# Optimization experiments

Measured on AMD Instinct MI355X. Metric: run time of the kernel, lower is better.

The kernel has to match this reference:

```python
import jax, jax.numpy as jnp
import numpy as np
import math

P, DD, N, E, NDRUGS = 256, 128, 1024, 250000, 200000
BASELINE = 6.0

def _prelu(x, a):
    return jnp.where(x >= 0, x, a * x)

def _lrelu(x):
    return jnp.where(x >= 0, x, 0.2 * x)

def _lin(x, W, b):
    return x @ W.T + b

def setup_inputs() -> dict:
    key = jax.random.key(0)
    ks = jax.random.split(key, 40)
    f32 = jnp.float32
    inp = {}
    inp["target_features"] = jax.random.normal(ks[0], (P,), f32)
    inp["form_features"] = jax.random.normal(ks[1], (N, P), f32)
    inp["role_features"] = jax.random.normal(ks[2], (N, P), f32)
    inp["form_neighbors"] = jnp.arange(N, dtype=jnp.int32)
    inp["form_binds_src"] = jax.random.randint(ks[3], (E,), 0, N, jnp.int32)
    inp["form_binds_dst"] = jax.random.randint(ks[4], (E,), 0, NDRUGS, jnp.int32)
    inp["form_binds_y"] = jax.random.uniform(ks[5], (E,), f32, 4.0, 9.0)
    inp["role_neighbors"] = jnp.arange(N, dtype=jnp.int32)
    inp["role_binds_src"] = jax.random.randint(ks[6], (E,), 0, N, jnp.int32)
    inp["role_binds_dst"] = jax.random.randint(ks[7], (E,), 0, NDRUGS, jnp.int32)
    inp["role_binds_y"] = jax.random.uniform(ks[8], (E,), f32, 4.0, 9.0)
    inp["drug_features"] = jax.random.normal(ks[9], (NDRUGS, DD), f32)
    s = 0.02
    # prot_refiner: Linear(P,P) -> PReLU -> Linear(P,P)
    inp["Wr1"] = jax.random.normal(ks[10], (P, P), f32) * s
    inp["br1"] = jnp.zeros((P,), f32)
    inp["ar1"] = jnp.asarray(0.25, f32)
    inp["Wr2"] = jax.random.normal(ks[11], (P, P), f32) * s
    inp["br2"] = jnp.zeros((P,), f32)
    # q/k/v projections
    inp["Wq"] = jax.random.normal(ks[12], (DD, P), f32) * s
    inp["bq"] = jnp.zeros((DD,), f32)
    inp["Wk"] = jax.random.normal(ks[13], (DD, DD), f32) * s
    inp["bk"] = jnp.zeros((DD,), f32)
    inp["Wv"] = jax.random.normal(ks[14], (DD, DD), f32) * s
    inp["bv"] = jnp.zeros((DD,), f32)
    inp["layer_emb"] = jax.random.normal(ks[15], (2, 16), f32) * s
    # attn_net: (2P+16)->128->64->1 with LeakyReLU(0.2)
    inp["Wa1"] = jax.random.normal(ks[16], (128, 2 * P + 16), f32) * s
    inp["ba1"] = jnp.zeros((128,), f32)
    inp["Wa2"] = jax.random.normal(ks[17], (64, 128), f32) * s
    inp["ba2"] = jnp.zeros((64,), f32)
    inp["Wa3"] = jax.random.normal(ks[18], (1, 64), f32) * s
    inp["ba3"] = jnp.zeros((1,), f32)
    # integration_mlp: Linear(DD,P) -> PReLU -> Linear(P,P)
    inp["Wi1"] = jax.random.normal(ks[19], (P, DD), f32) * s
    inp["bi1"] = jnp.zeros((P,), f32)
    inp["ai"] = jnp.asarray(0.25, f32)
    inp["Wi2"] = jax.random.normal(ks[20], (P, P), f32) * s
    inp["bi2"] = jnp.zeros((P,), f32)
    inp["ln_g"] = jnp.ones((P,), f32)
    inp["ln_b"] = jnp.zeros((P,), f32)
    return inp

def reference(target_features, form_features, role_features, form_neighbors,
              form_binds_src, form_binds_dst, form_binds_y,
              role_neighbors, role_binds_src, role_binds_dst, role_binds_y,
              drug_features,
              Wr1, br1, ar1, Wr2, br2, Wq, bq, Wk, bk, Wv, bv, layer_emb,
              Wa1, ba1, Wa2, ba2, Wa3, ba3, Wi1, bi1, ai, Wi2, bi2, ln_g, ln_b):
    def refine(x):
        return _lin(_prelu(_lin(x, Wr1, br1), ar1), Wr2, br2)

    zt = refine(target_features)          # [P]
    zf = refine(form_features)            # [N, P]
    zr = refine(role_features)            # [N, P]
    Qv = _lin(zt, Wq, bq)                 # [DD]

    def build_msgs(neighbors, src, dst, y):
        # segment id for each edge: position of src in (sorted) neighbor_ids;
        # edges whose src is not a neighbor go to the dummy segment n.
        n = neighbors.shape[0]
        pos = jnp.clip(jnp.searchsorted(neighbors, src), 0, n - 1)
        seg = jnp.where(neighbors[pos] == src, pos, n)
        d = drug_features[dst]                                # [E, DD] gather
        K = _lin(d, Wk, bk)                                   # [E, DD]
        V = _lin(d, Wv, bv) * (y - BASELINE)[:, None]         # [E, DD]
        s = (K @ Qv) / math.sqrt(DD)                          # [E]
        nseg = n + 1
        m = jax.ops.segment_max(s, seg, num_segments=nseg)    # per-neighbor max
        ex = jnp.exp(s - m[seg])                              # stable softmax numerator
        den = jax.ops.segment_sum(ex, seg, num_segments=nseg)[:n]          # [N]
        num = jax.ops.segment_sum(ex[:, None] * V, seg, num_segments=nseg)[:n]  # [N, DD]
        return jnp.where(den[:, None] > 0, num / jnp.maximum(den, 1e-30)[:, None], 0.0)

    form_msgs = build_msgs(form_neighbors, form_binds_src, form_binds_dst, form_binds_y)
    role_msgs = build_msgs(role_neighbors, role_binds_src, role_binds_dst, role_binds_y)

    def attn(zn, layer_id):
        n = zn.shape[0]
        le = jnp.broadcast_to(layer_emb[layer_id], (n, 16))
        zt_e = jnp.broadcast_to(zt, (n, P))
        x = jnp.concatenate([zt_e, zn, le], axis=-1)          # [N, 2P+16]
        h = _lrelu(_lin(x, Wa1, ba1))
        h = _lrelu(_lin(h, Wa2, ba2))
        return _lin(h, Wa3, ba3)                              # [N, 1]

    all_msgs = jnp.concatenate([form_msgs, role_msgs], axis=0)   # [2N, DD]
    all_attn = jnp.concatenate([attn(zf, 0), attn(zr, 1)], axis=0)  # [2N, 1]
    w = jax.nn.softmax(all_attn, axis=0)
    v_prior = jnp.sum(w * all_msgs, axis=0)                   # [DD]
    integ = _lin(_prelu(_lin(v_prior, Wi1, bi1), ai), Wi2, bi2)
    x = zt + integ
    mu = jnp.mean(x, axis=-1, keepdims=True)
    var = jnp.var(x, axis=-1, keepdims=True)
    z = (x - mu) / jnp.sqrt(var + 1e-5) * ln_g + ln_b
    return (z, form_msgs, role_msgs)
```

## Files before the change

kernel.cpp:

```cpp
#include <hip/hip_runtime.h>

#define NP 256
#define NDD 128
#define NN 1024
#define NE 250000
#define SB 62
#define RB 129

__global__ __launch_bounds__(256) void refine_qk_hist_kernel(
    const float* __restrict__ tgt, const float* __restrict__ formf, const float* __restrict__ rolef,
    const float* __restrict__ Wr1, const float* __restrict__ br1, const float* __restrict__ ar1,
    const float* __restrict__ Wr2, const float* __restrict__ br2,
    const float* __restrict__ Wq, const float* __restrict__ bq,
    const float* __restrict__ Wk, const float* __restrict__ bk,
    const int* __restrict__ neighF, const int* __restrict__ srcF,
    const int* __restrict__ neighR, const int* __restrict__ srcR,
    float* __restrict__ zt, float* __restrict__ zf, float* __restrict__ zr,
    float* __restrict__ qk, float* __restrict__ s0,
    int* __restrict__ count)
{
  __shared__ float X[16][NP];
  __shared__ float H[16][NP];
  __shared__ float Zs[NP];
  __shared__ float Q[NDD];
  __shared__ float red[NDD];
  const int t = threadIdx.x;

  if (blockIdx.x >= RB){
    int bi = blockIdx.x - RB;
    int role = bi >= SB ? 1 : 0;
    int blk = bi - role*SB;
    const int* neigh = role ? neighR : neighF;
    const int* src   = role ? srcR   : srcF;
    int* cnt = count + role*NN;
    int* NB = (int*)&X[0][0];
    int* lh = NB + NN;
    #pragma unroll
    for (int i = 0; i < NN/256; i++){
      NB[t + i*256] = neigh[t + i*256];
      lh[t + i*256] = 0;
    }
    __syncthreads();
    #pragma unroll
    for (int i = 0; i < 16; i++){
      int e = blk*4096 + i*256 + t;
      if (e < NE){
        int s = src[e];
        int pos;
        if ((unsigned)s < NN && NB[s] == s) pos = s;
        else {
          int lo = 0, hi = NN;
          while (lo < hi){ int mid = (lo+hi)>>1; if (NB[mid] < s) lo = mid+1; else hi = mid; }
          pos = lo < NN ? lo : NN-1;
        }
        if (NB[pos] == s) atomicAdd(&lh[pos], 1);
      }
    }
    __syncthreads();
    #pragma unroll
    for (int i = 0; i < NN/256; i++){
      int c = lh[t + i*256];
      if (c > 0) atomicAdd(&cnt[t + i*256], c);
    }
    return;
  }

  const int base = blockIdx.x * 16;
  #pragma unroll
  for (int r = 0; r < 16; r++){
    int row = base + r;
    if (row < 2*NN + 1){
      const float* xp;
      if (row == 0)        xp = tgt;
      else if (row <= NN)  xp = formf + (size_t)(row-1)*NP;
      else                 xp = rolef + (size_t)(row-NN-1)*NP;
      X[r][t] = xp[t];
    } else {
      X[r][t] = 0.f;
    }
  }
  __syncthreads();
  const float a1 = ar1[0];
  float acc[16];
  #pragma unroll
  for (int r = 0; r < 16; r++) acc[r] = 0.f;
  const float4* w1p = reinterpret_cast<const float4*>(Wr1) + t*(NP/4);
  for (int k4 = 0; k4 < NP/4; k4++){
    float4 w = w1p[k4];
    #pragma unroll
    for (int r = 0; r < 16; r++){
      float4 xv = *reinterpret_cast<const float4*>(&X[r][k4*4]);
      acc[r] = fmaf(w.x, xv.x, acc[r]);
      acc[r] = fmaf(w.y, xv.y, acc[r]);
      acc[r] = fmaf(w.z, xv.z, acc[r]);
      acc[r] = fmaf(w.w, xv.w, acc[r]);
    }
  }
  const float b1 = br1[t];
  #pragma unroll
  for (int r = 0; r < 16; r++){
    float h = acc[r] + b1;
    H[r][t] = h >= 0.f ? h : a1*h;
  }
  __syncthreads();
  #pragma unroll
  for (int r = 0; r < 16; r++) acc[r] = 0.f;
  const float4* w2p = reinterpret_cast<const float4*>(Wr2) + t*(NP/4);
  for (int k4 = 0; k4 < NP/4; k4++){
    float4 w = w2p[k4];
    #pragma unroll
    for (int r = 0; r < 16; r++){
      float4 hv = *reinterpret_cast<const float4*>(&H[r][k4*4]);
      acc[r] = fmaf(w.x, hv.x, acc[r]);
      acc[r] = fmaf(w.y, hv.y, acc[r]);
      acc[r] = fmaf(w.z, hv.z, acc[r]);
      acc[r] = fmaf(w.w, hv.w, acc[r]);
    }
  }
  const float b2 = br2[t];
  #pragma unroll
  for (int r = 0; r < 16; r++){
    int row = base + r;
    if (row < 2*NN + 1){
      float v = acc[r] + b2;
      float* op;
      if (row == 0){ op = zt; Zs[t] = v; }
      else if (row <= NN)  op = zf + (size_t)(row-1)*NP;
      else                 op = zr + (size_t)(row-NN-1)*NP;
      op[t] = v;
    }
  }

  if (blockIdx.x == 0){
    __syncthreads();
    if (t < NDD){
      float a = 0.f;
      const float4* wq = reinterpret_cast<const float4*>(Wq) + t*(NP/4);
      for (int k4 = 0; k4 < NP/4; k4++){
        float4 w = wq[k4];
        float4 zv = *reinterpret_cast<const float4*>(&Zs[k4*4]);
        a = fmaf(w.x, zv.x, fmaf(w.y, zv.y, fmaf(w.z, zv.z, fmaf(w.w, zv.w, a))));
      }
      float qv = a + bq[t];
      Q[t] = qv;
      red[t] = bk[t] * qv;
    }
    __syncthreads();
    const float rs = 0.08838834764831845f;
    if (t < NDD){
      float a2 = 0.f;
      for (int j = 0; j < NDD; j++) a2 = fmaf(Wk[j*NDD + t], Q[j], a2);
      qk[t] = a2 * rs;
    }
    for (int o = 64; o; o >>= 1){
      if (t < o) red[t] += red[t+o];
      __syncthreads();
    }
    if (t == 0) s0[0] = red[0] * rs;
  }
}

__device__ __forceinline__ int seg_of(const int* NB, int s){
  if ((unsigned)s < NN && NB[s] == s) return s;
  int lo = 0, hi = NN;
  while (lo < hi){ int mid = (lo+hi)>>1; if (NB[mid] < s) lo = mid+1; else hi = mid; }
  return lo < NN ? lo : NN-1;
}

__global__ __launch_bounds__(1024) void scatter_kernel(
    const int* __restrict__ neighF, const int* __restrict__ srcF,
    const int* __restrict__ dstF, const float* __restrict__ yF,
    const int* __restrict__ neighR, const int* __restrict__ srcR,
    const int* __restrict__ dstR, const float* __restrict__ yR,
    const int* __restrict__ count, int* __restrict__ cursor0,
    int* __restrict__ offsets, int2* __restrict__ edges)
{
  __shared__ int NB[NN];
  __shared__ int lcur[NN];
  __shared__ int sscan[NN];
  __shared__ int obase[NN];
  __shared__ int lbase[NN];
  int bi = blockIdx.x;
  int role = bi >= SB ? 1 : 0;
  int blk = bi - role*SB;
  const int* neigh = role ? neighR : neighF;
  const int* src   = role ? srcR   : srcF;
  const int* dst   = role ? dstR   : dstF;
  const float* yb  = role ? yR     : yF;
  int* cur0 = cursor0 + role*NN;
  int2* ed  = edges   + (size_t)role*NE;
  int t = threadIdx.x;
  NB[t] = neigh[t];
  lcur[t] = 0;
  int c0 = count[role*NN + t];
  sscan[t] = c0;
  __syncthreads();
  for (int o = 1; o < NN; o <<= 1){
    int v = (t >= o) ? sscan[t-o] : 0;
    __syncthreads();
    sscan[t] += v;
    __syncthreads();
  }
  obase[t] = sscan[t] - c0;
  if (blk == 0) offsets[role*NN + t] = sscan[t] - c0;
  __syncthreads();

  int segr[4], locr[4]; int2 edr[4];
  #pragma unroll
  for (int i = 0; i < 4; i++){
    int e = blk*4096 + i*1024 + t;
    segr[i] = -1;
    if (e < NE){
      int s = src[e];
      int pos = seg_of(NB, s);
      if (NB[pos] == s){
        segr[i] = pos;
        edr[i]  = make_int2(dst[e], __float_as_int(yb[e]));
        locr[i] = atomicAdd(&lcur[pos], 1);
      }
    }
  }
  __syncthreads();
  int c = lcur[t];
  if (c > 0) lbase[t] = obase[t] + atomicAdd(&cur0[t], c);
  __syncthreads();
  #pragma unroll
  for (int i = 0; i < 4; i++){
    if (segr[i] >= 0){
      ed[(size_t)(lbase[segr[i]] + locr[i])] = edr[i];
    }
  }
}

__global__ __launch_bounds__(256) void seg_kernel(
    const float* __restrict__ drug,
    const int2* __restrict__ edges,
    const int* __restrict__ offsets, const int* __restrict__ count,
    const float* __restrict__ qk, const float* __restrict__ s0p,
    float* __restrict__ g, float* __restrict__ den, float* __restrict__ cfac)
{
  int b = blockIdx.x;
  int tid = threadIdx.x;
  int w = tid >> 6, lane = tid & 63, l32 = lane & 31, half = lane >> 5;
  int off = offsets[b], cnt = count[b];
  int l = b >> 10;
  const int2* eb = edges + (size_t)l*NE;
  float4 q = reinterpret_cast<const float4*>(qk)[l32];
  float s0 = s0p[0];
  int chunk = (cnt + 3) >> 2;
  int start = w*chunk;
  int end = min(start + chunk, cnt);
  float dn = 0.f, cc = 0.f;
  float4 ga = make_float4(0.f,0.f,0.f,0.f);
  for (int i = start; i < end; i += 8){
    int dstp[4]; float yp[4]; bool vp[4];
    #pragma unroll
    for (int p2 = 0; p2 < 4; p2++){
      int idx = i + 2*p2 + half;
      bool v = idx < end;
      int2 e = eb[off + (v ? idx : start)];
      dstp[p2] = e.x; yp[p2] = __int_as_float(e.y); vp[p2] = v;
    }
    float4 dv[4];
    #pragma unroll
    for (int p2 = 0; p2 < 4; p2++){
      dv[p2] = reinterpret_cast<const float4*>(drug + (size_t)dstp[p2]*NDD)[l32];
    }
    #pragma unroll
    for (int p2 = 0; p2 < 4; p2++){
      float4 d = dv[p2];
      float s = fmaf(d.x, q.x, fmaf(d.y, q.y, fmaf(d.z, q.z, d.w*q.w)));
      s += __shfl_xor(s, 16, 64);
      s += __shfl_xor(s,  8, 64);
      s += __shfl_xor(s,  4, 64);
      s += __shfl_xor(s,  2, 64);
      s += __shfl_xor(s,  1, 64);
      float ex = vp[p2] ? __expf(s + s0) : 0.f;
      float wv = ex * (yp[p2] - 6.0f);
      dn += ex; cc += wv;
      ga.x = fmaf(wv, d.x, ga.x);
      ga.y = fmaf(wv, d.y, ga.y);
      ga.z = fmaf(wv, d.z, ga.z);
      ga.w = fmaf(wv, d.w, ga.w);
    }
  }
  __shared__ float4 sG[8][32];
  __shared__ float sD[8], sC[8];
  int slot = w*2 + half;
  sG[slot][l32] = ga;
  if (l32 == 0){ sD[slot] = dn; sC[slot] = cc; }
  __syncthreads();
  if (tid < NDD){
    int a = tid >> 2, c = tid & 3;
    float v = 0.f;
    #pragma unroll
    for (int k = 0; k < 8; k++)
      v += reinterpret_cast<const float*>(&sG[k][a])[c];
    g[(size_t)b*NDD + tid] = v;
    if (tid == 0){
      float ds = 0.f, cs = 0.f;
      #pragma unroll
      for (int k = 0; k < 8; k++){ ds += sD[k]; cs += sC[k]; }
      den[b] = ds; cfac[b] = cs;
    }
  }
}

__global__ __launch_bounds__(256) void attn_msgs_kernel(
    const float* __restrict__ zt, const float* __restrict__ zf, const float* __restrict__ zr,
    const float* __restrict__ lemb,
    const float* __restrict__ Wa1, const float* __restrict__ ba1,
    const float* __restrict__ Wa2, const float* __restrict__ ba2,
    const float* __restrict__ Wa3, const float* __restrict__ ba3,
    const float* __restrict__ g, const float* __restrict__ den, const float* __restrict__ cfac,
    const float* __restrict__ Wv, const float* __restrict__ bv,
    float* __restrict__ attn, float* __restrict__ msgsf, float* __restrict__ outm)
{
  int t = threadIdx.x;
  int tt = t & 127, grp = t >> 7;
  if (blockIdx.x < 256){
    __shared__ float X[8][528];
    __shared__ float H1[8][NDD];
    int base = blockIdx.x*8;
    for (int r = 0; r < 8; r++){
      int i = base + r;
      int layer = i >> 10, nn = i & (NN-1);
      const float* zn = (layer == 0) ? (zf + (size_t)nn*NP) : (zr + (size_t)nn*NP);
      for (int idx = t; idx < 528; idx += 256){
        float v;
        if (idx < NP)        v = zt[idx];
        else if (idx < 2*NP) v = zn[idx - NP];
        else                 v = lemb[layer*16 + (idx - 2*NP)];
        X[r][idx] = v;
      }
    }
    __syncthreads();
    float acc[4];
    #pragma unroll
    for (int r = 0; r < 4; r++) acc[r] = 0.f;
    const float4* w1 = reinterpret_cast<const float4*>(Wa1) + tt*(528/4);
    for (int k4 = 0; k4 < 132; k4++){
      float4 w = w1[k4];
      #pragma unroll
      for (int r = 0; r < 4; r++){
        float4 xv = *reinterpret_cast<const float4*>(&X[grp*4 + r][k4*4]);
        acc[r] = fmaf(w.x, xv.x, acc[r]);
        acc[r] = fmaf(w.y, xv.y, acc[r]);
        acc[r] = fmaf(w.z, xv.z, acc[r]);
        acc[r] = fmaf(w.w, xv.w, acc[r]);
      }
    }
    float b1 = ba1[tt];
    #pragma unroll
    for (int r = 0; r < 4; r++){
      float h = acc[r] + b1;
      H1[grp*4 + r][tt] = h >= 0.f ? h : 0.2f*h;
    }
    __syncthreads();
    if (tt < 64){
      float acc2[4];
      #pragma unroll
      for (int r = 0; r < 4; r++) acc2[r] = 0.f;
      const float4* w2 = reinterpret_cast<const float4*>(Wa2) + tt*(NDD/4);
      for (int k4 = 0; k4 < NDD/4; k4++){
        float4 w = w2[k4];
        #pragma unroll
        for (int r = 0; r < 4; r++){
          float4 hv = *reinterpret_cast<const float4*>(&H1[grp*4 + r][k4*4]);
          acc2[r] = fmaf(w.x, hv.x, acc2[r]);
          acc2[r] = fmaf(w.y, hv.y, acc2[r]);
          acc2[r] = fmaf(w.z, hv.z, acc2[r]);
          acc2[r] = fmaf(w.w, hv.w, acc2[r]);
        }
      }
      float b2 = ba2[tt];
      float w3 = Wa3[tt];
      float b3 = ba3[0];
      #pragma unroll
      for (int r = 0; r < 4; r++){
        float h = acc2[r] + b2;
        h = h >= 0.f ? h : 0.2f*h;
        float p = w3 * h;
        #pragma unroll
        for (int o = 32; o; o >>= 1) p += __shfl_xor(p, o, 64);
        if (tt == 0) attn[base + grp*4 + r] = p + b3;
      }
    }
  } else {
    __shared__ float G[8][NDD];
    int base = (blockIdx.x - 256)*8;
    #pragma unroll
    for (int r = 0; r < 4; r++) G[grp*4 + r][tt] = g[(size_t)(base + grp*4 + r)*NDD + tt];
    __syncthreads();
    float acc[4];
    #pragma unroll
    for (int r = 0; r < 4; r++) acc[r] = 0.f;
    const float4* wv4 = reinterpret_cast<const float4*>(Wv) + tt*(NDD/4);
    for (int k4 = 0; k4 < NDD/4; k4++){
      float4 w = wv4[k4];
      #pragma unroll
      for (int r = 0; r < 4; r++){
        float4 gv = *reinterpret_cast<const float4*>(&G[grp*4 + r][k4*4]);
        acc[r] = fmaf(w.x, gv.x, acc[r]);
        acc[r] = fmaf(w.y, gv.y, acc[r]);
        acc[r] = fmaf(w.z, gv.z, acc[r]);
        acc[r] = fmaf(w.w, gv.w, acc[r]);
      }
    }
    float bvj = bv[tt];
    #pragma unroll
    for (int r = 0; r < 4; r++){
      int row = base + grp*4 + r;
      float dn = den[row];
      float v = 0.f;
      if (dn > 0.f) v = (acc[r] + bvj*cfac[row]) / fmaxf(dn, 1e-30f);
      msgsf[(size_t)row*NDD + tt] = v;
      outm [(size_t)row*NDD + tt] = v;
    }
  }
}

__global__ __launch_bounds__(1024) void vprior_final_kernel(
    const float* __restrict__ attn, const float* __restrict__ msgsf,
    const float* __restrict__ zt,
    const float* __restrict__ Wi1, const float* __restrict__ bi1, const float* __restrict__ ai,
    const float* __restrict__ Wi2, const float* __restrict__ bi2,
    const float* __restrict__ ln_g, const float* __restrict__ ln_b,
    float* __restrict__ zout)
{
  __shared__ float A[2*NN];
  __shared__ float red[1024];
  __shared__ float Pp[8][NDD];
  __shared__ float V[NDD];
  __shared__ float T1[NP];
  __shared__ float red2[NP];
  int t = threadIdx.x;
  A[t] = attn[t]; A[t+1024] = attn[t+1024];
  __syncthreads();
  float mx = fmaxf(A[t], A[t+1024]);
  red[t] = mx; __syncthreads();
  for (int o = 512; o; o >>= 1){ if (t < o) red[t] = fmaxf(red[t], red[t+o]); __syncthreads(); }
  float M = red[0]; __syncthreads();
  float sm = __expf(A[t] - M) + __expf(A[t+1024] - M);
  red[t] = sm; __syncthreads();
  for (int o = 512; o; o >>= 1){ if (t < o) red[t] += red[t+o]; __syncthreads(); }
  float inv = 1.f / red[0]; __syncthreads();
  A[t]      = __expf(A[t]      - M) * inv;
  A[t+1024] = __expf(A[t+1024] - M) * inv;
  __syncthreads();
  int j = t & 127, grp = t >> 7;
  float acc = 0.f;
  int i0 = grp * 256;
  for (int i = i0; i < i0 + 256; i++) acc = fmaf(A[i], msgsf[(size_t)i*NDD + j], acc);
  Pp[grp][j] = acc;
  __syncthreads();
  if (t < NDD){
    float v = 0.f;
    #pragma unroll
    for (int gg = 0; gg < 8; gg++) v += Pp[gg][t];
    V[t] = v;
  }
  __syncthreads();
  float x = 0.f;
  if (t < NP){
    float a1 = 0.f;
    const float4* w1 = reinterpret_cast<const float4*>(Wi1) + t*(NDD/4);
    for (int k4 = 0; k4 < NDD/4; k4++){
      float4 w = w1[k4];
      float4 vv = *reinterpret_cast<const float4*>(&V[k4*4]);
      a1 = fmaf(w.x, vv.x, fmaf(w.y, vv.y, fmaf(w.z, vv.z, fmaf(w.w, vv.w, a1))));
    }
    float h = a1 + bi1[t];
    float a = ai[0];
    T1[t] = h >= 0.f ? h : a*h;
  }
  __syncthreads();
  if (t < NP){
    float a2 = 0.f;
    const float4* w2 = reinterpret_cast<const float4*>(Wi2) + t*(NP/4);
    for (int k4 = 0; k4 < NP/4; k4++){
      float4 w = w2[k4];
      float4 hv = *reinterpret_cast<const float4*>(&T1[k4*4]);
      a2 = fmaf(w.x, hv.x, fmaf(w.y, hv.y, fmaf(w.z, hv.z, fmaf(w.w, hv.w, a2))));
    }
    x = zt[t] + a2 + bi2[t];
    red2[t] = x;
  }
  __syncthreads();
  for (int o = 128; o; o >>= 1){ if (t < o) red2[t] += red2[t+o]; __syncthreads(); }
  float mu = red2[0] * (1.f/256.f); __syncthreads();
  float d = x - mu;
  if (t < NP) red2[t] = d*d;
  __syncthreads();
  for (int o = 128; o; o >>= 1){ if (t < o) red2[t] += red2[t+o]; __syncthreads(); }
  if (t < NP){
    float var = red2[0] * (1.f/256.f);
    float zz = d * rsqrtf(var + 1e-5f) * ln_g[t] + ln_b[t];
    zout[t] = zz;
  }
}

extern "C" void kernel_launch(void* const* d_in, const int* in_sizes, int n_in,
                              void* d_out, int out_size, void* d_ws, size_t ws_size,
                              hipStream_t stream)
{
  const float* tgt    = (const float*)d_in[0];
  const float* formf  = (const float*)d_in[1];
  const float* rolef  = (const float*)d_in[2];
  const int* fneigh   = (const int*)d_in[3];
  const int* fsrc     = (const int*)d_in[4];
  const int* fdst     = (const int*)d_in[5];
  const float* fy     = (const float*)d_in[6];
  const int* rneigh   = (const int*)d_in[7];
  const int* rsrc     = (const int*)d_in[8];
  const int* rdst     = (const int*)d_in[9];
  const float* ry     = (const float*)d_in[10];
  const float* drug   = (const float*)d_in[11];
  const float* Wr1 = (const float*)d_in[12];
  const float* br1 = (const float*)d_in[13];
  const float* ar1 = (const float*)d_in[14];
  const float* Wr2 = (const float*)d_in[15];
  const float* br2 = (const float*)d_in[16];
  const float* Wq  = (const float*)d_in[17];
  const float* bq  = (const float*)d_in[18];
  const float* Wk  = (const float*)d_in[19];
  const float* bk  = (const float*)d_in[20];
  const float* Wv  = (const float*)d_in[21];
  const float* bv  = (const float*)d_in[22];
  const float* lemb= (const float*)d_in[23];
  const float* Wa1 = (const float*)d_in[24];
  const float* ba1 = (const float*)d_in[25];
  const float* Wa2 = (const float*)d_in[26];
  const float* ba2 = (const float*)d_in[27];
  const float* Wa3 = (const float*)d_in[28];
  const float* ba3 = (const float*)d_in[29];
  const float* Wi1 = (const float*)d_in[30];
  const float* bi1 = (const float*)d_in[31];
  const float* ai  = (const float*)d_in[32];
  const float* Wi2 = (const float*)d_in[33];
  const float* bi2 = (const float*)d_in[34];
  const float* lng = (const float*)d_in[35];
  const float* lnb = (const float*)d_in[36];
  (void)in_sizes; (void)n_in; (void)out_size; (void)ws_size;

  float* ws = (float*)d_ws;
  float* zt_     = ws + 0;
  float* zf_     = ws + 256;
  float* zr_     = ws + 262400;
  float* qk_     = ws + 524544;
  float* s0_     = ws + 524672;
  float* attn_   = ws + 524800;
  float* den_    = ws + 527104;
  float* cfac_   = ws + 529152;
  float* g_      = ws + 531200;
  float* msgsf_  = ws + 793344;
  int*   count_  = (int*)(ws + 1055488);
  int*   offs_   = (int*)(ws + 1057536);
  int*   cursor_ = (int*)(ws + 1059584);
  int2*  edges_  = (int2*)(ws + 1061632);

  hipMemsetAsync(count_, 0, 3*2*NN*sizeof(int), stream);

  refine_qk_hist_kernel<<<RB + 2*SB, 256, 0, stream>>>(
      tgt, formf, rolef, Wr1, br1, ar1, Wr2, br2, Wq, bq, Wk, bk,
      fneigh, fsrc, rneigh, rsrc,
      zt_, zf_, zr_, qk_, s0_, count_);

  scatter_kernel<<<2*SB, 1024, 0, stream>>>(fneigh, fsrc, fdst, fy,
                                            rneigh, rsrc, rdst, ry,
                                            count_, cursor_, offs_, edges_);

  seg_kernel<<<2*NN, 256, 0, stream>>>(drug, edges_, offs_, count_, qk_, s0_,
                                       g_, den_, cfac_);

  attn_msgs_kernel<<<512, 256, 0, stream>>>(zt_, zf_, zr_, lemb,
                                            Wa1, ba1, Wa2, ba2, Wa3, ba3,
                                            g_, den_, cfac_, Wv, bv,
                                            attn_, msgsf_, (float*)d_out + NP);
  vprior_final_kernel<<<1, 1024, 0, stream>>>(attn_, msgsf_, zt_,
                                              Wi1, bi1, ai, Wi2, bi2,
                                              lng, lnb, (float*)d_out);
}
```

Measured before the change: 390.8 us.

## Transpose weights in a prep kernel and hoist constant attention-input terms

```diff
diff --git a/kernel.cpp b/kernel.cpp
--- a/kernel.cpp
+++ b/kernel.cpp
@@ -5,29 +5,66 @@
 #define NN 1024
 #define NE 250000
 #define SB 62
-#define RB 129
+#define RB2 257
+
+__global__ __launch_bounds__(256) void prep_kernel(
+    const float* __restrict__ Wr1, const float* __restrict__ Wr2,
+    const float* __restrict__ Wa1, const float* __restrict__ Wa2,
+    const float* __restrict__ Wv,
+    float* __restrict__ Wr1T, float* __restrict__ Wr2T,
+    float* __restrict__ Wa1mT, float* __restrict__ Wa2T, float* __restrict__ WvT)
+{
+  __shared__ float T[64][65];
+  int b = blockIdx.x, t = threadIdx.x;
+  const float* src; float* dst;
+  int sC, sr0, sc0, dC, dr0, dc0;
+  if (b < 16){        int ti=b;    src=Wr1; sC=256; sr0=(ti/4)*64; sc0=(ti%4)*64;
+                      dst=Wr1T; dC=256; dr0=sc0; dc0=sr0; }
+  else if (b < 32){   int ti=b-16; src=Wr2; sC=256; sr0=(ti/4)*64; sc0=(ti%4)*64;
+                      dst=Wr2T; dC=256; dr0=sc0; dc0=sr0; }
+  else if (b < 40){   int ti=b-32; src=Wa1; sC=528; sr0=(ti/4)*64; sc0=256+(ti%4)*64;
+                      dst=Wa1mT; dC=128; dr0=(ti%4)*64; dc0=sr0; }
+  else if (b < 42){   int ti=b-40; src=Wa2; sC=128; sr0=0; sc0=ti*64;
+                      dst=Wa2T; dC=64; dr0=sc0; dc0=0; }
+  else {              int ti=b-42; src=Wv;  sC=128; sr0=(ti/2)*64; sc0=(ti%2)*64;
+                      dst=WvT; dC=128; dr0=sc0; dc0=sr0; }
+  #pragma unroll
+  for (int j = 0; j < 16; j++){
+    int idx = t + j*256;
+    int r = idx >> 6, c = idx & 63;
+    T[c][r] = src[(size_t)(sr0 + r)*sC + sc0 + c];
+  }
+  __syncthreads();
+  #pragma unroll
+  for (int j = 0; j < 16; j++){
+    int idx = t + j*256;
+    int r = idx >> 6, c = idx & 63;
+    dst[(size_t)(dr0 + r)*dC + dc0 + c] = T[r][c];
+  }
+}
 
 __global__ __launch_bounds__(256) void refine_qk_hist_kernel(
     const float* __restrict__ tgt, const float* __restrict__ formf, const float* __restrict__ rolef,
-    const float* __restrict__ Wr1, const float* __restrict__ br1, const float* __restrict__ ar1,
-    const float* __restrict__ Wr2, const float* __restrict__ br2,
+    const float* __restrict__ Wr1T, const float* __restrict__ br1, const float* __restrict__ ar1,
+    const float* __restrict__ Wr2T, const float* __restrict__ br2,
     const float* __restrict__ Wq, const float* __restrict__ bq,
     const float* __restrict__ Wk, const float* __restrict__ bk,
+    const float* __restrict__ Wa1, const float* __restrict__ ba1, const float* __restrict__ lemb,
     const int* __restrict__ neighF, const int* __restrict__ srcF,
     const int* __restrict__ neighR, const int* __restrict__ srcR,
     float* __restrict__ zt, float* __restrict__ zf, float* __restrict__ zr,
-    float* __restrict__ qk, float* __restrict__ s0,
+    float* __restrict__ qk, float* __restrict__ s0, float* __restrict__ cl,
     int* __restrict__ count)
 {
-  __shared__ float X[16][NP];
-  __shared__ float H[16][NP];
+  __shared__ float X[8][NP];
+  __shared__ float H[8][NP];
   __shared__ float Zs[NP];
   __shared__ float Q[NDD];
   __shared__ float red[NDD];
   const int t = threadIdx.x;
 
-  if (blockIdx.x >= RB){
-    int bi = blockIdx.x - RB;
+  if (blockIdx.x >= RB2){
+    int bi = blockIdx.x - RB2;
     int role = bi >= SB ? 1 : 0;
     int blk = bi - role*SB;
     const int* neigh = role ? neighR : neighF;
@@ -65,9 +102,9 @@
     return;
   }
 
-  const int base = blockIdx.x * 16;
-  #pragma unroll
-  for (int r = 0; r < 16; r++){
+  const int base = blockIdx.x * 8;
+  #pragma unroll
+  for (int r = 0; r < 8; r++){
     int row = base + r;
     if (row < 2*NN + 1){
       const float* xp;
@@ -81,45 +118,49 @@
   }
   __syncthreads();
   const float a1 = ar1[0];
-  float acc[16];
-  #pragma unroll
-  for (int r = 0; r < 16; r++) acc[r] = 0.f;
-  const float4* w1p = reinterpret_cast<const float4*>(Wr1) + t*(NP/4);
-  for (int k4 = 0; k4 < NP/4; k4++){
-    float4 w = w1p[k4];
-    #pragma unroll
-    for (int r = 0; r < 16; r++){
-      float4 xv = *reinterpret_cast<const float4*>(&X[r][k4*4]);
-      acc[r] = fmaf(w.x, xv.x, acc[r]);
-      acc[r] = fmaf(w.y, xv.y, acc[r]);
-      acc[r] = fmaf(w.z, xv.z, acc[r]);
-      acc[r] = fmaf(w.w, xv.w, acc[r]);
+  float acc[8];
+  #pragma unroll
+  for (int r = 0; r < 8; r++) acc[r] = 0.f;
+  for (int k = 0; k < NP; k += 4){
+    float w0 = Wr1T[(k+0)*NP + t];
+    float w1 = Wr1T[(k+1)*NP + t];
+    float w2 = Wr1T[(k+2)*NP + t];
+    float w3 = Wr1T[(k+3)*NP + t];
+    #pragma unroll
+    for (int r = 0; r < 8; r++){
+      float4 x = *reinterpret_cast<const float4*>(&X[r][k]);
+      acc[r] = fmaf(w0, x.x, acc[r]);
+      acc[r] = fmaf(w1, x.y, acc[r]);
+      acc[r] = fmaf(w2, x.z, acc[r]);
+      acc[r] = fmaf(w3, x.w, acc[r]);
     }
   }
   const float b1 = br1[t];
   #pragma unroll
-  for (int r = 0; r < 16; r++){
+  for (int r = 0; r < 8; r++){
     float h = acc[r] + b1;
     H[r][t] = h >= 0.f ? h : a1*h;
   }
   __syncthreads();
   #pragma unroll
-  for (int r = 0; r < 16; r++) acc[r] = 0.f;
-  const float4* w2p = reinterpret_cast<const float4*>(Wr2) + t*(NP/4);
-  for (int k4 = 0; k4 < NP/4; k4++){
-    float4 w = w2p[k4];
-    #pragma unroll
-    for (int r = 0; r < 16; r++){
-      float4 hv = *reinterpret_cast<const float4*>(&H[r][k4*4]);
-      acc[r] = fmaf(w.x, hv.x, acc[r]);
-      acc[r] = fmaf(w.y, hv.y, acc[r]);
-      acc[r] = fmaf(w.z, hv.z, acc[r]);
-      acc[r] = fmaf(w.w, hv.w, acc[r]);
+  for (int r = 0; r < 8; r++) acc[r] = 0.f;
+  for (int k = 0; k < NP; k += 4){
+    float w0 = Wr2T[(k+0)*NP + t];
+    float w1 = Wr2T[(k+1)*NP + t];
+    float w2 = Wr2T[(k+2)*NP + t];
+    float w3 = Wr2T[(k+3)*NP + t];
+    #pragma unroll
+    for (int r = 0; r < 8; r++){
+      float4 h4 = *reinterpret_cast<const float4*>(&H[r][k]);
+      acc[r] = fmaf(w0, h4.x, acc[r]);
+      acc[r] = fmaf(w1, h4.y, acc[r]);
+      acc[r] = fmaf(w2, h4.z, acc[r]);
+      acc[r] = fmaf(w3, h4.w, acc[r]);
     }
   }
   const float b2 = br2[t];
   #pragma unroll
-  for (int r = 0; r < 16; r++){
+  for (int r = 0; r < 8; r++){
     int row = base + r;
     if (row < 2*NN + 1){
       float v = acc[r] + b2;
@@ -157,6 +198,21 @@
       __syncthreads();
     }
     if (t == 0) s0[0] = red[0] * rs;
+    {
+      int l = t >> 7, tt = t & 127;
+      const float4* wrow = reinterpret_cast<const float4*>(Wa1 + (size_t)tt*528);
+      float a = 0.f;
+      for (int k4 = 0; k4 < 64; k4++){
+        float4 w = wrow[k4];
+        float4 zv = *reinterpret_cast<const float4*>(&Zs[k4*4]);
+        a = fmaf(w.x, zv.x, fmaf(w.y, zv.y, fmaf(w.z, zv.z, fmaf(w.w, zv.w, a))));
+      }
+      const float* wle = Wa1 + (size_t)tt*528 + 512;
+      const float* le = lemb + l*16;
+      #pragma unroll
+      for (int j = 0; j < 16; j++) a = fmaf(wle[j], le[j], a);
+      cl[l*NDD + tt] = a + ba1[tt];
+    }
   }
 }
 
@@ -307,83 +363,82 @@
 }
 
 __global__ __launch_bounds__(256) void attn_msgs_kernel(
-    const float* __restrict__ zt, const float* __restrict__ zf, const float* __restrict__ zr,
-    const float* __restrict__ lemb,
-    const float* __restrict__ Wa1, const float* __restrict__ ba1,
-    const float* __restrict__ Wa2, const float* __restrict__ ba2,
+    const float* __restrict__ zf, const float* __restrict__ zr,
+    const float* __restrict__ cl,
+    const float* __restrict__ Wa1mT,
+    const float* __restrict__ Wa2T, const float* __restrict__ ba2,
     const float* __restrict__ Wa3, const float* __restrict__ ba3,
     const float* __restrict__ g, const float* __restrict__ den, const float* __restrict__ cfac,
-    const float* __restrict__ Wv, const float* __restrict__ bv,
+    const float* __restrict__ WvT, const float* __restrict__ bv,
     float* __restrict__ attn, float* __restrict__ msgsf, float* __restrict__ outm)
 {
   int t = threadIdx.x;
   int tt = t & 127, grp = t >> 7;
   if (blockIdx.x < 256){
-    __shared__ float X[8][528];
+    __shared__ float Zn[8][NP];
     __shared__ float H1[8][NDD];
     int base = blockIdx.x*8;
+    int layer = blockIdx.x >> 7;
+    const float* zsrc = layer ? zr : zf;
+    #pragma unroll
     for (int r = 0; r < 8; r++){
-      int i = base + r;
-      int layer = i >> 10, nn = i & (NN-1);
-      const float* zn = (layer == 0) ? (zf + (size_t)nn*NP) : (zr + (size_t)nn*NP);
-      for (int idx = t; idx < 528; idx += 256){
-        float v;
-        if (idx < NP)        v = zt[idx];
-        else if (idx < 2*NP) v = zn[idx - NP];
-        else                 v = lemb[layer*16 + (idx - 2*NP)];
-        X[r][idx] = v;
-      }
+      int nn = (base + r) & (NN-1);
+      Zn[r][t] = zsrc[(size_t)nn*NP + t];
     }
     __syncthreads();
     float acc[4];
     #pragma unroll
     for (int r = 0; r < 4; r++) acc[r] = 0.f;
-    const float4* w1 = reinterpret_cast<const float4*>(Wa1) + tt*(528/4);
-    for (int k4 = 0; k4 < 132; k4++){
-      float4 w = w1[k4];
+    for (int k = 0; k < NP; k += 4){
+      float w0 = Wa1mT[(k+0)*NDD + tt];
+      float w1 = Wa1mT[(k+1)*NDD + tt];
+      float w2 = Wa1mT[(k+2)*NDD + tt];
+      float w3 = Wa1mT[(k+3)*NDD + tt];
       #pragma unroll
       for (int r = 0; r < 4; r++){
-        float4 xv = *reinterpret_cast<const float4*>(&X[grp*4 + r][k4*4]);
-        acc[r] = fmaf(w.x, xv.x, acc[r]);
-        acc[r] = fmaf(w.y, xv.y, acc[r]);
-        acc[r] = fmaf(w.z, xv.z, acc[r]);
-        acc[r] = fmaf(w.w, xv.w, acc[r]);
-      }
-    }
-    float b1 = ba1[tt];
+        float4 x = *reinterpret_cast<const float4*>(&Zn[grp*4 + r][k]);
+        acc[r] = fmaf(w0, x.x, acc[r]);
+        acc[r] = fmaf(w1, x.y, acc[r]);
+        acc[r] = fmaf(w2, x.z, acc[r]);
+        acc[r] = fmaf(w3, x.w, acc[r]);
+      }
+    }
+    float c1 = cl[layer*NDD + tt];
     #pragma unroll
     for (int r = 0; r < 4; r++){
-      float h = acc[r] + b1;
+      float h = acc[r] + c1;
       H1[grp*4 + r][tt] = h >= 0.f ? h : 0.2f*h;
     }
     __syncthreads();
-    if (tt < 64){
-      float acc2[4];
+    if (t < 64){
+      float acc2[8];
       #pragma unroll
-      for (int r = 0; r < 4; r++) acc2[r] = 0.f;
-      const float4* w2 = reinterpret_cast<const float4*>(Wa2) + tt*(NDD/4);
-      for (int k4 = 0; k4 < NDD/4; k4++){
-        float4 w = w2[k4];
+      for (int r = 0; r < 8; r++) acc2[r] = 0.f;
+      for (int k = 0; k < NDD; k += 4){
+        float w0 = Wa2T[(k+0)*64 + t];
+        float w1 = Wa2T[(k+1)*64 + t];
+        float w2 = Wa2T[(k+2)*64 + t];
+        float w3 = Wa2T[(k+3)*64 + t];
         #pragma unroll
-        for (int r = 0; r < 4; r++){
-          float4 hv = *reinterpret_cast<const float4*>(&H1[grp*4 + r][k4*4]);
-          acc2[r] = fmaf(w.x, hv.x, acc2[r]);
-          acc2[r] = fmaf(w.y, hv.y, acc2[r]);
-          acc2[r] = fmaf(w.z, hv.z, acc2[r]);
-          acc2[r] = fmaf(w.w, hv.w, acc2[r]);
+        for (int r = 0; r < 8; r++){
+          float4 h4 = *reinterpret_cast<const float4*>(&H1[r][k]);
+          acc2[r] = fmaf(w0, h4.x, acc2[r]);
+          acc2[r] = fmaf(w1, h4.y, acc2[r]);
+          acc2[r] = fmaf(w2, h4.z, acc2[r]);
+          acc2[r] = fmaf(w3, h4.w, acc2[r]);
         }
       }
-      float b2 = ba2[tt];
-      float w3 = Wa3[tt];
+      float b2 = ba2[t];
+      float w3v = Wa3[t];
       float b3 = ba3[0];
       #pragma unroll
-      for (int r = 0; r < 4; r++){
+      for (int r = 0; r < 8; r++){
         float h = acc2[r] + b2;
         h = h >= 0.f ? h : 0.2f*h;
-        float p = w3 * h;
+        float p = w3v * h;
         #pragma unroll
         for (int o = 32; o; o >>= 1) p += __shfl_xor(p, o, 64);
-        if (tt == 0) attn[base + grp*4 + r] = p + b3;
+        if (t == 0) attn[base + r] = p + b3;
       }
     }
   } else {
@@ -395,16 +450,18 @@
     float acc[4];
     #pragma unroll
     for (int r = 0; r < 4; r++) acc[r] = 0.f;
-    const float4* wv4 = reinterpret_cast<const float4*>(Wv) + tt*(NDD/4);
-    for (int k4 = 0; k4 < NDD/4; k4++){
-      float4 w = wv4[k4];
+    for (int k = 0; k < NDD; k += 4){
+      float w0 = WvT[(k+0)*NDD + tt];
+      float w1 = WvT[(k+1)*NDD + tt];
+      float w2 = WvT[(k+2)*NDD + tt];
+      float w3 = WvT[(k+3)*NDD + tt];
       #pragma unroll
       for (int r = 0; r < 4; r++){
-        float4 gv = *reinterpret_cast<const float4*>(&G[grp*4 + r][k4*4]);
-        acc[r] = fmaf(w.x, gv.x, acc[r]);
-        acc[r] = fmaf(w.y, gv.y, acc[r]);
-        acc[r] = fmaf(w.z, gv.z, acc[r]);
-        acc[r] = fmaf(w.w, gv.w, acc[r]);
+        float4 gv = *reinterpret_cast<const float4*>(&G[grp*4 + r][k]);
+        acc[r] = fmaf(w0, gv.x, acc[r]);
+        acc[r] = fmaf(w1, gv.y, acc[r]);
+        acc[r] = fmaf(w2, gv.z, acc[r]);
+        acc[r] = fmaf(w3, gv.w, acc[r]);
       }
     }
     float bvj = bv[tt];
@@ -549,7 +606,8 @@
   float* zr_     = ws + 262400;
   float* qk_     = ws + 524544;
   float* s0_     = ws + 524672;
-  float* attn_   = ws + 524800;
+  float* cl_     = ws + 524800;
+  float* attn_   = ws + 525056;
   float* den_    = ws + 527104;
   float* cfac_   = ws + 529152;
   float* g_      = ws + 531200;
@@ -558,13 +616,22 @@
   int*   offs_   = (int*)(ws + 1057536);
   int*   cursor_ = (int*)(ws + 1059584);
   int2*  edges_  = (int2*)(ws + 1061632);
+  float* Wr1T_   = ws + 3061632;
+  float* Wr2T_   = ws + 3127168;
+  float* Wa1mT_  = ws + 3192704;
+  float* Wa2T_   = ws + 3225472;
+  float* WvT_    = ws + 3233664;
 
   hipMemsetAsync(count_, 0, 3*2*NN*sizeof(int), stream);
 
-  refine_qk_hist_kernel<<<RB + 2*SB, 256, 0, stream>>>(
-      tgt, formf, rolef, Wr1, br1, ar1, Wr2, br2, Wq, bq, Wk, bk,
+  prep_kernel<<<46, 256, 0, stream>>>(Wr1, Wr2, Wa1, Wa2, Wv,
+                                      Wr1T_, Wr2T_, Wa1mT_, Wa2T_, WvT_);
+
+  refine_qk_hist_kernel<<<RB2 + 2*SB, 256, 0, stream>>>(
+      tgt, formf, rolef, Wr1T_, br1, ar1, Wr2T_, br2, Wq, bq, Wk, bk,
+      Wa1, ba1, lemb,
       fneigh, fsrc, rneigh, rsrc,
-      zt_, zf_, zr_, qk_, s0_, count_);
+      zt_, zf_, zr_, qk_, s0_, cl_, count_);
 
   scatter_kernel<<<2*SB, 1024, 0, stream>>>(fneigh, fsrc, fdst, fy,
                                             rneigh, rsrc, rdst, ry,
@@ -573,9 +640,9 @@
   seg_kernel<<<2*NN, 256, 0, stream>>>(drug, edges_, offs_, count_, qk_, s0_,
                                        g_, den_, cfac_);
 
-  attn_msgs_kernel<<<512, 256, 0, stream>>>(zt_, zf_, zr_, lemb,
-                                            Wa1, ba1, Wa2, ba2, Wa3, ba3,
-                                            g_, den_, cfac_, Wv, bv,
+  attn_msgs_kernel<<<512, 256, 0, stream>>>(zf_, zr_, cl_,
+                                            Wa1mT_, Wa2T_, ba2, Wa3, ba3,
+                                            g_, den_, cfac_, WvT_, bv,
                                             attn_, msgsf_, (float*)d_out + NP);
   vprior_final_kernel<<<1, 1024, 0, stream>>>(attn_, msgsf_, zt_,
                                               Wi1, bi1, ai, Wi2, bi2,
```

After: 368.4 us. 5.7% less time.
